# Kernel tuning notes

Measured on AMD Instinct MI355X. Metric: run time of the kernel, lower is better.

## Reference

```python
import jax, jax.numpy as jnp
import numpy as np

NUM_HEADS = 12
EPSILON = 1e-6
SCORE_SCALE = 1.0


def setup_inputs() -> dict:
    key = jax.random.key(0)
    ks = jax.random.split(key, 5)
    B, L, E = 2, 2048, 768
    x = jax.random.normal(ks[0], (B, L, E), dtype=jnp.float32)
    attention_mask = jnp.ones((B, L), dtype=jnp.int32)
    # linear params (lecun-ish scale)
    Wqkv = jax.random.normal(ks[1], (E, 3 * E), dtype=jnp.float32) / np.sqrt(E)
    bqkv = jnp.zeros((3 * E,), dtype=jnp.float32)
    Wout = jax.random.normal(ks[2], (E, E), dtype=jnp.float32) / np.sqrt(E)
    bout = jnp.zeros((E,), dtype=jnp.float32)
    return {"x": x, "attention_mask": attention_mask, "Wqkv": Wqkv,
            "bqkv": bqkv, "Wout": Wout, "bout": bout}


def reference(x, attention_mask, Wqkv, bqkv, Wout, bout):
    B, L, E = x.shape
    H = NUM_HEADS
    D = E // H
    qkv = x @ Wqkv + bqkv                      # [B,L,3E]
    q, k, v = jnp.split(qkv, 3, axis=-1)
    q = q.reshape(B, L, H, D).transpose(0, 2, 1, 3)  # [B,H,L,D]
    k = k.reshape(B, L, H, D).transpose(0, 2, 1, 3)
    v = v.reshape(B, L, H, D).transpose(0, 2, 1, 3)

    dot = jnp.einsum('bhid,bhjd->bhij', q, k)        # [B,H,L,L]
    q_sq = jnp.sum(q * q, axis=-1)[..., :, None]     # [B,H,L,1]
    k_sq = jnp.sum(k * k, axis=-1)[..., None, :]     # [B,H,1,L]
    scores = (dot * dot) / (q_sq + k_sq - 2.0 * dot + EPSILON)
    scores = scores * SCORE_SCALE

    pad = attention_mask[:, None, None, :]           # [B,1,1,L]
    scores = jnp.where(pad == 1, scores, jnp.finfo(scores.dtype).min)

    attn = jax.nn.softmax(scores, axis=-1)
    out = jnp.einsum('bhij,bhjd->bhid', attn, v)     # [B,H,L,D]
    out = out.transpose(0, 2, 1, 3).reshape(B, L, E)
    return out @ Wout + bout
```

## Files before the change

kernel.cpp:

```cpp
#include <hip/hip_runtime.h>
#include <hip/hip_bf16.h>
#include <cstdint>
#include <cstddef>


typedef __bf16 bf16_t;
typedef __bf16 bf16x8 __attribute__((ext_vector_type(8)));
typedef __bf16 bf16x4 __attribute__((ext_vector_type(4)));
typedef float floatx4 __attribute__((ext_vector_type(4)));
typedef _Float16 half_t;
typedef _Float16 half4 __attribute__((ext_vector_type(4)));

#define DEVI static __device__ __forceinline__

#define Bc 2
#define Lc 2048
#define Ec 768
#define Hc 12
#define Dc 64
#define N3c 2304
#define Mc 4096
#define ROWSc (Bc * Hc * Lc)

DEVI void glds16(const bf16_t* g, bf16_t* l) {
  __builtin_amdgcn_global_load_lds(
      (const __attribute__((address_space(1))) void*)g,
      (__attribute__((address_space(3))) void*)l, 16, 0, 0);
}

#define NBCVT 3072
#define NBTC1 1728
#define NBTC2 576

__global__ __launch_bounds__(256) void k_prep(
    const float* __restrict__ x, bf16_t* __restrict__ xb,
    const float* __restrict__ Wqkv, bf16_t* __restrict__ WqT,
    const float* __restrict__ Wout, bf16_t* __restrict__ WoT) {
  const int bid = blockIdx.x, tid = threadIdx.x;
  if (bid < NBCVT) {
    const int i = (bid * 256 + tid) * 4;
    float4 v = *(const float4*)(x + i);
    bf16x4 o;
    o[0] = (bf16_t)v.x; o[1] = (bf16_t)v.y; o[2] = (bf16_t)v.z; o[3] = (bf16_t)v.w;
    *(bf16x4*)(xb + i) = o;
    return;
  }
  __shared__ float tile[32][33];
  const float* in; bf16_t* out; int C, bx, by;
  if (bid < NBCVT + NBTC1) {
    const int r = bid - NBCVT;
    in = Wqkv; out = WqT; C = N3c; bx = r % 72; by = r / 72;
  } else {
    const int r = bid - NBCVT - NBTC1;
    in = Wout; out = WoT; C = Ec; bx = r % 24; by = r / 24;
  }
  const int R = Ec;
  const int c0 = bx * 32, r0 = by * 32;
  const int tx = tid & 31, ty = tid >> 5;
  #pragma unroll
  for (int i = 0; i < 32; i += 8)
    tile[ty + i][tx] = in[(size_t)(r0 + ty + i) * C + c0 + tx];
  __syncthreads();
  #pragma unroll
  for (int i = 0; i < 32; i += 8)
    out[(size_t)(c0 + ty + i) * R + r0 + tx] = (bf16_t)tile[tx][ty + i];
}


DEVI void gemm_core(const bf16_t* __restrict__ A, const bf16_t* __restrict__ Bt,
                    bf16_t* lA, bf16_t* lB, int m0, int n0, floatx4 (&acc)[4][4]) {
  const int tid = threadIdx.x, wave = tid >> 6, lane = tid & 63;
  const int wm = (wave >> 1) * 64, wn = (wave & 1) * 64;
  const int lrow = lane >> 2, lseg = lane & 3;
  const int quad = lane >> 4, r16 = lane & 15;
  for (int kk = 0; kk < 768; kk += 32) {
    glds16(A  + (size_t)(m0 + wave * 32      + lrow) * 768 + kk + lseg * 8, lA + (wave * 32) * 32);
    glds16(A  + (size_t)(m0 + wave * 32 + 16 + lrow) * 768 + kk + lseg * 8, lA + (wave * 32 + 16) * 32);
    glds16(Bt + (size_t)(n0 + wave * 32      + lrow) * 768 + kk + lseg * 8, lB + (wave * 32) * 32);
    glds16(Bt + (size_t)(n0 + wave * 32 + 16 + lrow) * 768 + kk + lseg * 8, lB + (wave * 32 + 16) * 32);
    __syncthreads();
    bf16x8 af[4], bv[4];
    #pragma unroll
    for (int mi = 0; mi < 4; mi++)
      af[mi] = *(const bf16x8*)(lA + (wm + mi * 16 + r16) * 32 + quad * 8);
    #pragma unroll
    for (int ni = 0; ni < 4; ni++)
      bv[ni] = *(const bf16x8*)(lB + (wn + ni * 16 + r16) * 32 + quad * 8);
    #pragma unroll
    for (int mi = 0; mi < 4; mi++)
      #pragma unroll
      for (int ni = 0; ni < 4; ni++)
        acc[mi][ni] = __builtin_amdgcn_mfma_f32_16x16x32_bf16(af[mi], bv[ni], acc[mi][ni], 0, 0, 0);
    __syncthreads();
  }
}

__global__ __launch_bounds__(256) void k_gemm_qkv(
    const bf16_t* __restrict__ A, const bf16_t* __restrict__ Bt,
    const float* __restrict__ bias,
    bf16_t* __restrict__ Qo, bf16_t* __restrict__ Ko, bf16_t* __restrict__ VTo) {
  __shared__ bf16_t lA[128 * 32];
  __shared__ bf16_t lB[128 * 32];
  const int m0 = blockIdx.y * 128, n0 = blockIdx.x * 128;
  const int tid = threadIdx.x, wave = tid >> 6, lane = tid & 63;
  const int wm = (wave >> 1) * 64, wn = (wave & 1) * 64;
  const int quad = lane >> 4, r16 = lane & 15;
  floatx4 acc[4][4] = {};
  gemm_core(A, Bt, lA, lB, m0, n0, acc);

  const int sec = n0 / 768;
  if (sec == 2) {
    #pragma unroll
    for (int ni = 0; ni < 4; ni++) {
      const int n = n0 + wn + ni * 16 + r16;
      const int nn = n - 1536;
      const int h = nn >> 6, d = nn & 63;
      const float bvs = bias[n];
      #pragma unroll
      for (int mi = 0; mi < 4; mi++) {
        const int m = m0 + wm + mi * 16 + quad * 4;
        const int b = m >> 11, l = m & 2047;
        bf16x4 o;
        #pragma unroll
        for (int reg = 0; reg < 4; reg++) o[reg] = (bf16_t)(acc[mi][ni][reg] + bvs);
        *(bf16x4*)(VTo + ((size_t)(b * Hc + h) * Dc + d) * Lc + l) = o;
      }
    }
  } else {
    bf16_t* dst = (sec == 0) ? Qo : Ko;
    #pragma unroll
    for (int ni = 0; ni < 4; ni++) {
      const int n = n0 + wn + ni * 16 + r16;
      const int nn = n - sec * 768;
      const int h = nn >> 6, d = nn & 63;
      const float bvs = bias[n];
      #pragma unroll
      for (int mi = 0; mi < 4; mi++) {
        #pragma unroll
        for (int reg = 0; reg < 4; reg++) {
          const int m = m0 + wm + mi * 16 + quad * 4 + reg;
          const int b = m >> 11, l = m & 2047;
          const float v = acc[mi][ni][reg] + bvs;
          dst[(((size_t)(b * Hc + h)) * Lc + l) * Dc + d] = (bf16_t)v;
        }
      }
    }
  }
}

__global__ __launch_bounds__(256) void k_gemm_out(
    const bf16_t* __restrict__ A, const bf16_t* __restrict__ Bt,
    const float* __restrict__ bias, float* __restrict__ out) {
  __shared__ bf16_t lA[128 * 32];
  __shared__ bf16_t lB[128 * 32];
  const int m0 = blockIdx.y * 128, n0 = blockIdx.x * 128;
  const int tid = threadIdx.x, wave = tid >> 6, lane = tid & 63;
  const int wm = (wave >> 1) * 64, wn = (wave & 1) * 64;
  const int quad = lane >> 4, r16 = lane & 15;
  floatx4 acc[4][4] = {};
  gemm_core(A, Bt, lA, lB, m0, n0, acc);
  #pragma unroll
  for (int ni = 0; ni < 4; ni++) {
    const int n = n0 + wn + ni * 16 + r16;
    const float bvs = bias[n];
    #pragma unroll
    for (int mi = 0; mi < 4; mi++) {
      #pragma unroll
      for (int reg = 0; reg < 4; reg++) {
        const int m = m0 + wm + mi * 16 + quad * 4 + reg;
        out[(size_t)m * Ec + n] = acc[mi][ni][reg] + bvs;
      }
    }
  }
}

__global__ __launch_bounds__(256) void k_sq(const bf16_t* __restrict__ Q,
                                            const bf16_t* __restrict__ K,
                                            const int* __restrict__ mask,
                                            float* __restrict__ qsq, float* __restrict__ ksq) {
  const int row = blockIdx.x * 256 + threadIdx.x;
  const bf16x8* q = (const bf16x8*)(Q + (size_t)row * 64);
  const bf16x8* k = (const bf16x8*)(K + (size_t)row * 64);
  float sq = 0.f, sk = 0.f;
  #pragma unroll
  for (int c = 0; c < 8; c++) {
    bf16x8 vq = q[c], vk = k[c];
    #pragma unroll
    for (int j = 0; j < 8; j++) {
      float a = (float)vq[j]; sq += a * a;
      float b = (float)vk[j]; sk += b * b;
    }
  }
  const int bh = row >> 11, l = row & 2047;
  const int b = bh / Hc;
  const int mk = mask[b * Lc + l];
  qsq[row] = sq;
  ksq[row] = (mk == 1) ? (sk + 1e-6f) : -1e30f;
}

__global__ __launch_bounds__(256, 6) void k_attn(
    const bf16_t* __restrict__ Q, const bf16_t* __restrict__ K,
    const bf16_t* __restrict__ VT, const float* __restrict__ qsq,
    const float* __restrict__ ksq,
    half_t* __restrict__ Op, float* __restrict__ Mp, float* __restrict__ Lp,
    int nS) {
  __shared__ bf16_t lK[4096];
  __shared__ bf16_t lV[4096];
  __shared__ bf16_t lP[4][16 * 72];
  const int gid = blockIdx.x;
  const int s = blockIdx.y;
  const int bh = gid >> 5, qt = gid & 31;
  const int tid = threadIdx.x, wave = tid >> 6, lane = tid & 63;
  const int quad = lane >> 4, r16 = lane & 15;
  const int q0 = qt * 64 + wave * 16;
  const bf16_t* Qh = Q + ((size_t)bh * Lc) * Dc;
  const bf16_t* Kh = K + ((size_t)bh * Lc) * Dc;
  const bf16_t* VTh = VT + ((size_t)bh * Dc) * Lc;
  const float* qsqh = qsq + bh * Lc;
  const float* ksqh = ksq + bh * Lc;
  bf16_t* myP = &lP[wave][0];

  const int kt_lo = (32 * s) / nS * 64;
  const int kt_hi = (32 * (s + 1)) / nS * 64;
  const int nt = (kt_hi - kt_lo) >> 6;

  const int p0 = wave * 64 + lane;
  const int srow = p0 >> 3;
  const int sj = (p0 & 7) ^ (srow & 7);
  const bf16_t* kg0 = Kh + (size_t)(kt_lo + srow) * 64 + sj * 8;
  const bf16_t* kg1 = kg0 + 32 * 64;
  const bf16_t* vg0 = VTh + (size_t)srow * Lc + kt_lo + sj * 8;
  const bf16_t* vg1 = vg0 + 32 * Lc;
  const int ld0 = wave * 64 * 8, ld1 = (256 + wave * 64) * 8;

  const int sl0 = ((quad ^ (r16 & 7)) * 8);
  const int sl1 = sl0 ^ 32;

  bf16x8 qf0 = *(const bf16x8*)(Qh + (size_t)(q0 + r16) * 64 + quad * 8);
  bf16x8 qf1 = *(const bf16x8*)(Qh + (size_t)(q0 + r16) * 64 + 32 + quad * 8);
  const float qs = qsqh[q0 + r16];
  float mi = -1e30f, li = 0.f;
  floatx4 of[4] = {};

  for (int t = 0; t < nt; t++) {
    const int kt = kt_lo + t * 64;
    floatx4 qsk[4];
    #pragma unroll
    for (int c = 0; c < 4; c++)
      qsk[c] = qs + *(const floatx4*)(ksqh + kt + c * 16 + quad * 4);
    __syncthreads();
    glds16(kg0, &lK[ld0]);
    glds16(kg1, &lK[ld1]);
    glds16(vg0, &lV[ld0]);
    glds16(vg1, &lV[ld1]);
    kg0 += 4096; kg1 += 4096; vg0 += 64; vg1 += 64;
    __syncthreads();

    floatx4 dot[4];
    #pragma unroll
    for (int c = 0; c < 4; c++) {
      const int rbase = (c * 16 + r16) * 64;
      bf16x8 kf0 = *(const bf16x8*)(&lK[rbase + sl0]);
      bf16x8 kf1 = *(const bf16x8*)(&lK[rbase + sl1]);
      floatx4 a = {};
      a = __builtin_amdgcn_mfma_f32_16x16x32_bf16(kf0, qf0, a, 0, 0, 0);
      a = __builtin_amdgcn_mfma_f32_16x16x32_bf16(kf1, qf1, a, 0, 0, 0);
      dot[c] = a;
    }
    floatx4 sv4[4];
    floatx4 mx = {-1e30f, -1e30f, -1e30f, -1e30f};
    #pragma unroll
    for (int c = 0; c < 4; c++) {
      const floatx4 den = qsk[c] - 2.f * dot[c];
      const floatx4 num = dot[c] * dot[c];
      floatx4 sc;
      #pragma unroll
      for (int e = 0; e < 4; e++) {
        float v = num[e] * __builtin_amdgcn_rcpf(den[e]);
        sc[e] = (qsk[c][e] < 0.f) ? -1e30f : v;
        mx[e] = fmaxf(mx[e], sc[e]);
      }
      sv4[c] = sc;
    }
    float rmax = fmaxf(fmaxf(mx[0], mx[1]), fmaxf(mx[2], mx[3]));
    rmax = fmaxf(rmax, __shfl_xor(rmax, 16));
    rmax = fmaxf(rmax, __shfl_xor(rmax, 32));
    const float mnew = fmaxf(mi, rmax);
    if (__ballot(rmax > mi) != 0ull) {
      const float alpha = __expf(mi - mnew);
      #pragma unroll
      for (int t4 = 0; t4 < 4; t4++) {
        #pragma unroll
        for (int reg = 0; reg < 4; reg++) of[t4][reg] *= alpha;
      }
      li *= alpha;
      mi = mnew;
    }
    floatx4 ps4 = {};
    #pragma unroll
    for (int c = 0; c < 4; c++) {
      const floatx4 e4 = sv4[c] - mi;
      floatx4 p4;
      bf16x4 pk;
      #pragma unroll
      for (int e = 0; e < 4; e++) {
        p4[e] = __expf(e4[e]);
        pk[e] = (bf16_t)p4[e];
      }
      ps4 += p4;
      *(bf16x4*)(myP + r16 * 72 + c * 16 + quad * 4) = pk;
    }
    float psum = (ps4[0] + ps4[1]) + (ps4[2] + ps4[3]);
    psum += __shfl_xor(psum, 16);
    psum += __shfl_xor(psum, 32);
    li += psum;

    bf16x8 pf0 = *(const bf16x8*)(myP + r16 * 72 + quad * 8);
    bf16x8 pf1 = *(const bf16x8*)(myP + r16 * 72 + 32 + quad * 8);
    #pragma unroll
    for (int t4 = 0; t4 < 4; t4++) {
      const int rbase = (t4 * 16 + r16) * 64;
      bf16x8 vf0 = *(const bf16x8*)(&lV[rbase + sl0]);
      bf16x8 vf1 = *(const bf16x8*)(&lV[rbase + sl1]);
      of[t4] = __builtin_amdgcn_mfma_f32_16x16x32_bf16(vf0, pf0, of[t4], 0, 0, 0);
      of[t4] = __builtin_amdgcn_mfma_f32_16x16x32_bf16(vf1, pf1, of[t4], 0, 0, 0);
    }
  }
  const size_t idx = (size_t)s * ROWSc + (size_t)bh * Lc + q0 + r16;
  #pragma unroll
  for (int t4 = 0; t4 < 4; t4++) {
    half4 o;
    #pragma unroll
    for (int reg = 0; reg < 4; reg++) o[reg] = (half_t)of[t4][reg];
    *(half4*)(Op + idx * 64 + t4 * 16 + quad * 4) = o;
  }
  if (lane < 16) { Mp[idx] = mi; Lp[idx] = li; }
}

__global__ __launch_bounds__(256) void k_merge(
    const half_t* __restrict__ Op, const float* __restrict__ Mp,
    const float* __restrict__ Lp, bf16_t* __restrict__ AO, int nS) {
  const int t = blockIdx.x * 256 + threadIdx.x;
  const int row = t >> 4, dc = (t & 15) * 4;
  float mmax = -1e30f;
  for (int s = 0; s < nS; s++) mmax = fmaxf(mmax, Mp[(size_t)s * ROWSc + row]);
  float L = 0.f;
  float o0 = 0.f, o1 = 0.f, o2 = 0.f, o3 = 0.f;
  for (int s = 0; s < nS; s++) {
    const size_t idx = (size_t)s * ROWSc + row;
    const float w = __expf(Mp[idx] - mmax);
    L += w * Lp[idx];
    const half4 v = *(const half4*)(Op + idx * 64 + dc);
    o0 += w * (float)v[0]; o1 += w * (float)v[1];
    o2 += w * (float)v[2]; o3 += w * (float)v[3];
  }
  const float inv = (L > 0.f) ? __builtin_amdgcn_rcpf(L) : 0.f;
  const int bh = row >> 11, l = row & 2047;
  const int b = bh / Hc, h = bh - b * Hc;
  bf16x4 o;
  o[0] = (bf16_t)(o0 * inv); o[1] = (bf16_t)(o1 * inv);
  o[2] = (bf16_t)(o2 * inv); o[3] = (bf16_t)(o3 * inv);
  *(bf16x4*)(AO + ((size_t)(b * Lc + l)) * Ec + h * 64 + dc) = o;
}


extern "C" void kernel_launch(void* const* d_in, const int* in_sizes, int n_in,
                              void* d_out, int out_size, void* d_ws, size_t ws_size,
                              hipStream_t stream) {
  const float* x    = (const float*)d_in[0];
  const int*   mask = (const int*)d_in[1];
  const float* Wqkv = (const float*)d_in[2];
  const float* bqkv = (const float*)d_in[3];
  const float* Wout = (const float*)d_in[4];
  const float* bout = (const float*)d_in[5];
  float* out = (float*)d_out;

  auto al = [](size_t v) { return (v + 255) & ~(size_t)255; };
  char* ws = (char*)d_ws;
  size_t off = 0;
  auto carve = [&](size_t bytes) -> char* {
    char* p = ws + off;
    off += al(bytes);
    return p;
  };
  bf16_t* WoT = (bf16_t*)carve((size_t)Ec * Ec * 2);
  bf16_t* Qb  = (bf16_t*)carve((size_t)ROWSc * Dc * 2);
  bf16_t* Kb  = (bf16_t*)carve((size_t)ROWSc * Dc * 2);
  bf16_t* VTb = (bf16_t*)carve((size_t)ROWSc * Dc * 2);
  bf16_t* AOb = (bf16_t*)carve((size_t)Mc * Ec * 2);
  float*  qsq = (float*)carve((size_t)ROWSc * 4);
  float*  ksq = (float*)carve((size_t)ROWSc * 4);
  const size_t uni = off;
  bf16_t* xb  = (bf16_t*)(ws + uni);
  bf16_t* WqT = (bf16_t*)(ws + uni + al((size_t)Mc * Ec * 2));
  const size_t ph1 = al((size_t)Mc * Ec * 2) + al((size_t)N3c * Ec * 2);
  auto ph2 = [&](int S) {
    return al((size_t)S * ROWSc * Dc * 2) + 2 * al((size_t)S * ROWSc * 4);
  };
  int S = 2;
  for (int cand : {4, 3}) {
    size_t need = uni + (ph1 > ph2(cand) ? ph1 : ph2(cand));
    if (need <= ws_size) { S = cand; break; }
  }
  half_t* Op = (half_t*)(ws + uni);
  float*  Mp = (float*)(ws + uni + al((size_t)S * ROWSc * Dc * 2));
  float*  Lp = (float*)(ws + uni + al((size_t)S * ROWSc * Dc * 2) + al((size_t)S * ROWSc * 4));
  (void)in_sizes; (void)n_in; (void)out_size;

  k_prep<<<NBCVT + NBTC1 + NBTC2, 256, 0, stream>>>(x, xb, Wqkv, WqT, Wout, WoT);
  k_gemm_qkv<<<dim3(N3c / 128, Mc / 128), 256, 0, stream>>>(xb, WqT, bqkv, Qb, Kb, VTb);
  k_sq<<<ROWSc / 256, 256, 0, stream>>>(Qb, Kb, mask, qsq, ksq);
  k_attn<<<dim3(ROWSc / 64, S), 256, 0, stream>>>(Qb, Kb, VTb, qsq, ksq, Op, Mp, Lp, S);
  k_merge<<<ROWSc * 16 / 256, 256, 0, stream>>>(Op, Mp, Lp, AOb, S);
  k_gemm_out<<<dim3(Ec / 128, Mc / 128), 256, 0, stream>>>(AOb, WoT, bout, out);
}
```

Baseline: 223.4 us.

## Double-buffer K/V tiles and feed P to PV MFMA from registers in fp16

The attention kernel now double-buffers the K and V shared-memory tiles, prefetching the next tile with async global-to-LDS loads while computing the current one, and uses one barrier per iteration instead of two. V is stored as fp16 and the probability tile is kept in registers as fp16, feeding 16x16x16 f16 MFMAs directly, which removes the per-wave P round trip through LDS. This trades doubled LDS use, and therefore a lower occupancy hint (5 instead of 6), for hidden load latency and fewer LDS accesses. It also runs twice as many smaller MFMAs and changes V/P precision from bf16 to fp16.

```diff
diff --git a/kernel.cpp b/kernel.cpp
--- a/kernel.cpp
+++ b/kernel.cpp
@@ -22,7 +22,7 @@
 #define Mc 4096
 #define ROWSc (Bc * Hc * Lc)
 
-DEVI void glds16(const bf16_t* g, bf16_t* l) {
+DEVI void glds16(const void* g, void* l) {
   __builtin_amdgcn_global_load_lds(
       (const __attribute__((address_space(1))) void*)g,
       (__attribute__((address_space(3))) void*)l, 16, 0, 0);
@@ -98,7 +98,7 @@
 __global__ __launch_bounds__(256) void k_gemm_qkv(
     const bf16_t* __restrict__ A, const bf16_t* __restrict__ Bt,
     const float* __restrict__ bias,
-    bf16_t* __restrict__ Qo, bf16_t* __restrict__ Ko, bf16_t* __restrict__ VTo) {
+    bf16_t* __restrict__ Qo, bf16_t* __restrict__ Ko, half_t* __restrict__ VTo) {
   __shared__ bf16_t lA[128 * 32];
   __shared__ bf16_t lB[128 * 32];
   const int m0 = blockIdx.y * 128, n0 = blockIdx.x * 128;
@@ -120,10 +120,10 @@
       for (int mi = 0; mi < 4; mi++) {
         const int m = m0 + wm + mi * 16 + quad * 4;
         const int b = m >> 11, l = m & 2047;
-        bf16x4 o;
+        half4 o;
         #pragma unroll
-        for (int reg = 0; reg < 4; reg++) o[reg] = (bf16_t)(acc[mi][ni][reg] + bvs);
-        *(bf16x4*)(VTo + ((size_t)(b * Hc + h) * Dc + d) * Lc + l) = o;
+        for (int reg = 0; reg < 4; reg++) o[reg] = (half_t)(acc[mi][ni][reg] + bvs);
+        *(half4*)(VTo + ((size_t)(b * Hc + h) * Dc + d) * Lc + l) = o;
       }
     }
   } else {
@@ -198,15 +198,14 @@
   ksq[row] = (mk == 1) ? (sk + 1e-6f) : -1e30f;
 }
 
-__global__ __launch_bounds__(256, 6) void k_attn(
+__global__ __launch_bounds__(256, 5) void k_attn(
     const bf16_t* __restrict__ Q, const bf16_t* __restrict__ K,
-    const bf16_t* __restrict__ VT, const float* __restrict__ qsq,
+    const half_t* __restrict__ VT, const float* __restrict__ qsq,
     const float* __restrict__ ksq,
     half_t* __restrict__ Op, float* __restrict__ Mp, float* __restrict__ Lp,
     int nS) {
-  __shared__ bf16_t lK[4096];
-  __shared__ bf16_t lV[4096];
-  __shared__ bf16_t lP[4][16 * 72];
+  __shared__ bf16_t lK[2][4096];
+  __shared__ half_t lV[2][4096];
   const int gid = blockIdx.x;
   const int s = blockIdx.y;
   const int bh = gid >> 5, qt = gid & 31;
@@ -215,10 +214,9 @@
   const int q0 = qt * 64 + wave * 16;
   const bf16_t* Qh = Q + ((size_t)bh * Lc) * Dc;
   const bf16_t* Kh = K + ((size_t)bh * Lc) * Dc;
-  const bf16_t* VTh = VT + ((size_t)bh * Dc) * Lc;
+  const half_t* VTh = VT + ((size_t)bh * Dc) * Lc;
   const float* qsqh = qsq + bh * Lc;
   const float* ksqh = ksq + bh * Lc;
-  bf16_t* myP = &lP[wave][0];
 
   const int kt_lo = (32 * s) / nS * 64;
   const int kt_hi = (32 * (s + 1)) / nS * 64;
@@ -229,8 +227,8 @@
   const int sj = (p0 & 7) ^ (srow & 7);
   const bf16_t* kg0 = Kh + (size_t)(kt_lo + srow) * 64 + sj * 8;
   const bf16_t* kg1 = kg0 + 32 * 64;
-  const bf16_t* vg0 = VTh + (size_t)srow * Lc + kt_lo + sj * 8;
-  const bf16_t* vg1 = vg0 + 32 * Lc;
+  const half_t* vg0 = VTh + (size_t)srow * Lc + kt_lo + sj * 8;
+  const half_t* vg1 = vg0 + 32 * Lc;
   const int ld0 = wave * 64 * 8, ld1 = (256 + wave * 64) * 8;
 
   const int sl0 = ((quad ^ (r16 & 7)) * 8);
@@ -242,26 +240,34 @@
   float mi = -1e30f, li = 0.f;
   floatx4 of[4] = {};
 
+  glds16(kg0, &lK[0][ld0]);
+  glds16(kg1, &lK[0][ld1]);
+  glds16(vg0, &lV[0][ld0]);
+  glds16(vg1, &lV[0][ld1]);
+  kg0 += 4096; kg1 += 4096; vg0 += 64; vg1 += 64;
+  __syncthreads();
+
   for (int t = 0; t < nt; t++) {
+    const int cur = t & 1;
+    if (t + 1 < nt) {
+      const int nxt = cur ^ 1;
+      glds16(kg0, &lK[nxt][ld0]);
+      glds16(kg1, &lK[nxt][ld1]);
+      glds16(vg0, &lV[nxt][ld0]);
+      glds16(vg1, &lV[nxt][ld1]);
+      kg0 += 4096; kg1 += 4096; vg0 += 64; vg1 += 64;
+    }
     const int kt = kt_lo + t * 64;
     floatx4 qsk[4];
     #pragma unroll
     for (int c = 0; c < 4; c++)
       qsk[c] = qs + *(const floatx4*)(ksqh + kt + c * 16 + quad * 4);
-    __syncthreads();
-    glds16(kg0, &lK[ld0]);
-    glds16(kg1, &lK[ld1]);
-    glds16(vg0, &lV[ld0]);
-    glds16(vg1, &lV[ld1]);
-    kg0 += 4096; kg1 += 4096; vg0 += 64; vg1 += 64;
-    __syncthreads();
-
     floatx4 dot[4];
     #pragma unroll
     for (int c = 0; c < 4; c++) {
       const int rbase = (c * 16 + r16) * 64;
-      bf16x8 kf0 = *(const bf16x8*)(&lK[rbase + sl0]);
-      bf16x8 kf1 = *(const bf16x8*)(&lK[rbase + sl1]);
+      bf16x8 kf0 = *(const bf16x8*)(&lK[cur][rbase + sl0]);
+      bf16x8 kf1 = *(const bf16x8*)(&lK[cur][rbase + sl1]);
       floatx4 a = {};
       a = __builtin_amdgcn_mfma_f32_16x16x32_bf16(kf0, qf0, a, 0, 0, 0);
       a = __builtin_amdgcn_mfma_f32_16x16x32_bf16(kf1, qf1, a, 0, 0, 0);
@@ -296,35 +302,34 @@
       li *= alpha;
       mi = mnew;
     }
+    half4 pk[4];
     floatx4 ps4 = {};
     #pragma unroll
     for (int c = 0; c < 4; c++) {
       const floatx4 e4 = sv4[c] - mi;
       floatx4 p4;
-      bf16x4 pk;
       #pragma unroll
       for (int e = 0; e < 4; e++) {
         p4[e] = __expf(e4[e]);
-        pk[e] = (bf16_t)p4[e];
+        pk[c][e] = (half_t)p4[e];
       }
       ps4 += p4;
-      *(bf16x4*)(myP + r16 * 72 + c * 16 + quad * 4) = pk;
     }
     float psum = (ps4[0] + ps4[1]) + (ps4[2] + ps4[3]);
     psum += __shfl_xor(psum, 16);
     psum += __shfl_xor(psum, 32);
     li += psum;
-
-    bf16x8 pf0 = *(const bf16x8*)(myP + r16 * 72 + quad * 8);
-    bf16x8 pf1 = *(const bf16x8*)(myP + r16 * 72 + 32 + quad * 8);
     #pragma unroll
     for (int t4 = 0; t4 < 4; t4++) {
       const int rbase = (t4 * 16 + r16) * 64;
-      bf16x8 vf0 = *(const bf16x8*)(&lV[rbase + sl0]);
-      bf16x8 vf1 = *(const bf16x8*)(&lV[rbase + sl1]);
-      of[t4] = __builtin_amdgcn_mfma_f32_16x16x32_bf16(vf0, pf0, of[t4], 0, 0, 0);
-      of[t4] = __builtin_amdgcn_mfma_f32_16x16x32_bf16(vf1, pf1, of[t4], 0, 0, 0);
-    }
+      #pragma unroll
+      for (int c = 0; c < 4; c++) {
+        const int slot = (2 * c + (quad >> 1)) ^ (r16 & 7);
+        half4 va = *(const half4*)(&lV[cur][rbase + slot * 8 + (quad & 1) * 4]);
+        of[t4] = __builtin_amdgcn_mfma_f32_16x16x16f16(va, pk[c], of[t4], 0, 0, 0);
+      }
+    }
+    __syncthreads();
   }
   const size_t idx = (size_t)s * ROWSc + (size_t)bh * Lc + q0 + r16;
   #pragma unroll
@@ -386,7 +391,7 @@
   bf16_t* WoT = (bf16_t*)carve((size_t)Ec * Ec * 2);
   bf16_t* Qb  = (bf16_t*)carve((size_t)ROWSc * Dc * 2);
   bf16_t* Kb  = (bf16_t*)carve((size_t)ROWSc * Dc * 2);
-  bf16_t* VTb = (bf16_t*)carve((size_t)ROWSc * Dc * 2);
+  half_t* VTb = (half_t*)carve((size_t)ROWSc * Dc * 2);
   bf16_t* AOb = (bf16_t*)carve((size_t)Mc * Ec * 2);
   float*  qsq = (float*)carve((size_t)ROWSc * 4);
   float*  ksq = (float*)carve((size_t)ROWSc * 4);
```

Measured after the change: 225.4 us. About the same (+0.9%).
